# Kernel tuning notes

Measured on AMD Instinct MI355X. Metric: run time of the kernel, lower is better.

The kernel has to match this reference:

```python
import jax, jax.numpy as jnp
import numpy as np

NUM_HEADS = 32
NUM_KV_HEADS = 8
HEAD_DIM = 64
HIDDEN = 2048
EPS = 1e-05
ROPE_THETA = 1000000.0


def _rmsnorm(x, w):
    # x: [..., head_dim]
    var = jnp.mean(x * x, axis=-1, keepdims=True)
    return w * (x * jax.lax.rsqrt(var + EPS))


def _rope(q, k):
    # q,k: [B, h, T, d]
    T, d = q.shape[2], q.shape[3]
    inv_freq = 1.0 / (ROPE_THETA ** (jnp.arange(0, d, 2, dtype=jnp.float32) / d))
    t = jnp.arange(T, dtype=jnp.float32)
    freqs = jnp.outer(t, inv_freq)               # [T, d/2]
    emb = jnp.concatenate([freqs, freqs], -1)    # [T, d]
    cos = jnp.cos(emb)[None, None].astype(q.dtype)
    sin = jnp.sin(emb)[None, None].astype(q.dtype)

    def rotate(x):
        x1, x2 = x[..., : d // 2], x[..., d // 2 :]
        return jnp.concatenate([-x2, x1], -1)

    return q * cos + rotate(q) * sin, k * cos + rotate(k) * sin


def setup_inputs() -> dict:
    key = jax.random.key(0)
    ks = jax.random.split(key, 7)
    s = 0.02
    x = jax.random.normal(ks[0], (2, 2048, HIDDEN), jnp.float32)
    Wq = jax.random.normal(ks[1], (HIDDEN, NUM_HEADS * HEAD_DIM), jnp.float32) * s
    Wk = jax.random.normal(ks[2], (HIDDEN, NUM_KV_HEADS * HEAD_DIM), jnp.float32) * s
    Wv = jax.random.normal(ks[3], (HIDDEN, NUM_KV_HEADS * HEAD_DIM), jnp.float32) * s
    Wo = jax.random.normal(ks[4], (NUM_HEADS * HEAD_DIM, HIDDEN), jnp.float32) * s
    q_ln_w = jnp.ones((HEAD_DIM,), jnp.float32)
    k_ln_w = jnp.ones((HEAD_DIM,), jnp.float32)
    return {"x": x, "Wq": Wq, "Wk": Wk, "Wv": Wv, "Wo": Wo, "q_ln_w": q_ln_w, "k_ln_w": k_ln_w}


def reference(x, Wq, Wk, Wv, Wo, q_ln_w, k_ln_w):
    B, T, _ = x.shape
    g = NUM_HEADS // NUM_KV_HEADS  # GQA groups = 4
    q = (x @ Wq).reshape(B, T, NUM_HEADS, HEAD_DIM)
    k = (x @ Wk).reshape(B, T, NUM_KV_HEADS, HEAD_DIM)
    v = (x @ Wv).reshape(B, T, NUM_KV_HEADS, HEAD_DIM)
    q = _rmsnorm(q, q_ln_w)
    k = _rmsnorm(k, k_ln_w)
    q = q.transpose(0, 2, 1, 3)  # [B, nh, T, d]
    k = k.transpose(0, 2, 1, 3)  # [B, nkv, T, d]
    v = v.transpose(0, 2, 1, 3)
    q, k = _rope(q, k)
    # native GQA: fold query heads into (kv_head, group) without repeating K/V
    qg = q.reshape(B, NUM_KV_HEADS, g, T, HEAD_DIM)
    scale = 1.0 / jnp.sqrt(jnp.array(HEAD_DIM, q.dtype))
    scores = jnp.einsum("bkgtd,bksd->bkgts", qg, k) * scale  # [B,nkv,g,T,T]
    causal = jnp.tril(jnp.ones((T, T), bool))
    scores = jnp.where(causal, scores, jnp.finfo(scores.dtype).min)
    probs = jax.nn.softmax(scores, axis=-1)
    out = jnp.einsum("bkgts,bksd->bkgtd", probs, v)  # [B,nkv,g,T,d]
    out = out.reshape(B, NUM_HEADS, T, HEAD_DIM).transpose(0, 2, 1, 3).reshape(B, T, -1)
    return out @ Wo
```

## Files before the change

kernel.cpp:

```cpp
#include <hip/hip_runtime.h>
#include <cstdint>
#include <cstddef>

typedef unsigned short u16;
typedef __attribute__((ext_vector_type(8))) short short8;
typedef __attribute__((ext_vector_type(4))) short short4v;
typedef __attribute__((ext_vector_type(4))) float float4v;
typedef __attribute__((ext_vector_type(4))) unsigned short ushort4v;
typedef __attribute__((ext_vector_type(2))) float float2v;

__device__ __forceinline__ u16 f2bf(float f) {
    union { float f; uint32_t u; } x; x.f = f;
    uint32_t r = x.u + 0x7fffu + ((x.u >> 16) & 1u);
    return (u16)(r >> 16);
}
__device__ __forceinline__ float bf2f(u16 b) {
    union { uint32_t u; float f; } x; x.u = ((uint32_t)b) << 16;
    return x.f;
}
__device__ __forceinline__ uint32_t pack_bf16x2(float lo, float hi) {
    union { float f; uint32_t u; } a, b; a.f = lo; b.f = hi;
    return __builtin_amdgcn_perm(b.u + 0x8000u, a.u + 0x8000u, 0x07060302u);
}
__device__ __forceinline__ void gload_lds16(const u16* g, u16* l) {
    __builtin_amdgcn_global_load_lds(
        (const __attribute__((address_space(1))) void*)g,
        (__attribute__((address_space(3))) void*)l,
        16, 0, 0);
}

__global__ __launch_bounds__(256) void prep(const float4v* __restrict__ x,
                                            const float* __restrict__ Wq,
                                            const float* __restrict__ Wk,
                                            const float* __restrict__ Wv,
                                            const float* __restrict__ Wo,
                                            ushort4v* __restrict__ xb,
                                            u16* __restrict__ wqkv_t,
                                            u16* __restrict__ wo_t,
                                            float2v* __restrict__ tab) {
    __shared__ float lds[32][33];
    const int bid = blockIdx.x;
    const int tid = threadIdx.x;
    if (bid < 8192) {
        const int i = bid * 256 + tid;
        float4v v = x[i];
        ushort4v o;
        #pragma unroll
        for (int j = 0; j < 4; ++j) o[j] = f2bf(v[j]);
        xb[i] = o;
        return;
    }
    if (bid < 8448) {
        const int idx = (bid - 8192) * 256 + tid;
        const int t = idx >> 5;
        const int i = idx & 31;
        const float invf = exp2f(-(float)i * (19.931568569324174f / 32.0f));
        float sv, cv;
        sincosf((float)t * invf, &sv, &cv);
        float2v o; o[0] = cv; o[1] = sv;
        tab[idx] = o;
        return;
    }
    const float* src;
    int Ns, n0, k0, scol0;
    u16* dst;
    if (bid < 14592) {
        const int id = bid - 8448;
        const int bx = id % 96, by = id / 96;
        n0 = bx * 32; k0 = by * 32;
        if (n0 < 2048)      { src = Wq; Ns = 2048; scol0 = n0; }
        else if (n0 < 2560) { src = Wk; Ns = 512;  scol0 = n0 - 2048; }
        else                { src = Wv; Ns = 512;  scol0 = n0 - 2560; }
        dst = wqkv_t;
    } else {
        const int id = bid - 14592;
        const int bx = id & 63, by = id >> 6;
        n0 = bx * 32; k0 = by * 32;
        src = Wo; Ns = 2048; scol0 = n0;
        dst = wo_t;
    }
    const int row = tid >> 3;
    const int c4  = (tid & 7) * 4;
    const float4v v = *(const float4v*)(src + (size_t)(k0 + row) * Ns + scol0 + c4);
    #pragma unroll
    for (int i = 0; i < 4; ++i) lds[row][c4 + i] = v[i];
    __syncthreads();
    const int nrow = tid >> 3;
    const int k4   = (tid & 7) * 4;
    ushort4v o;
    #pragma unroll
    for (int i = 0; i < 4; ++i) o[i] = f2bf(lds[k4 + i][nrow]);
    *(ushort4v*)(dst + (size_t)(n0 + nrow) * 2048 + k0 + k4) = o;
}

__global__ __launch_bounds__(256) void gemm_bt(const u16* __restrict__ A,
                                               const u16* __restrict__ Bt,
                                               float* __restrict__ C,
                                               int M, int N, int K) {
    __shared__ u16 lds_a[128 * 32];
    __shared__ u16 lds_b[128 * 32];
    const int tid  = threadIdx.x;
    const int wave = tid >> 6;
    const int lane = tid & 63;
    const int quad = lane >> 4;
    const int l15  = lane & 15;
    const long m0 = (long)blockIdx.x * 128;
    const long n0 = (long)blockIdx.y * 128;
    const int wm = (wave >> 1) * 64;
    const int wn = (wave & 1) * 64;
    const int sa_row = lane >> 2;
    const int sa_col = (lane & 3) * 8;

    float4v acc[4][4];
    #pragma unroll
    for (int i = 0; i < 4; ++i)
        #pragma unroll
        for (int j = 0; j < 4; ++j)
            #pragma unroll
            for (int r = 0; r < 4; ++r) acc[i][j][r] = 0.0f;

    for (int k0 = 0; k0 < K; k0 += 32) {
        #pragma unroll
        for (int i = 0; i < 2; ++i) {
            const int slot = wave * 2 + i;
            const u16* ga = A  + (m0 + slot * 16 + sa_row) * (long)K + k0 + sa_col;
            gload_lds16(ga, lds_a + slot * 512);
            const u16* gb = Bt + (n0 + slot * 16 + sa_row) * (long)K + k0 + sa_col;
            gload_lds16(gb, lds_b + slot * 512);
        }
        __syncthreads();
        short8 af[4], bfr[4];
        #pragma unroll
        for (int mt = 0; mt < 4; ++mt)
            af[mt] = *(const short8*)(lds_a + (wm + mt * 16 + l15) * 32 + quad * 8);
        #pragma unroll
        for (int nt = 0; nt < 4; ++nt)
            bfr[nt] = *(const short8*)(lds_b + (wn + nt * 16 + l15) * 32 + quad * 8);
        #pragma unroll
        for (int mt = 0; mt < 4; ++mt)
            #pragma unroll
            for (int nt = 0; nt < 4; ++nt)
                acc[mt][nt] = __builtin_amdgcn_mfma_f32_16x16x32_bf16(af[mt], bfr[nt], acc[mt][nt], 0, 0, 0);
        __syncthreads();
    }
    #pragma unroll
    for (int mt = 0; mt < 4; ++mt) {
        #pragma unroll
        for (int nt = 0; nt < 4; ++nt) {
            const long gr = m0 + wm + mt * 16 + quad * 4;
            const long gc = n0 + wn + nt * 16 + l15;
            #pragma unroll
            for (int r = 0; r < 4; ++r)
                C[(gr + r) * N + gc] = acc[mt][nt][r];
        }
    }
}

__global__ __launch_bounds__(256) void gemm_qkv(const u16* __restrict__ A,
                                                const u16* __restrict__ Bt,
                                                const float* __restrict__ qw,
                                                const float* __restrict__ kw,
                                                const float2v* __restrict__ tab,
                                                u16* __restrict__ Qr,
                                                u16* __restrict__ Kr,
                                                u16* __restrict__ Vt) {
    const int K = 2048;
    __shared__ u16 lds_a[128 * 32];
    __shared__ u16 lds_b[128 * 32];
    const int tid  = threadIdx.x;
    const int wave = tid >> 6;
    const int lane = tid & 63;
    const int quad = lane >> 4;
    const int l15  = lane & 15;
    const long m0 = (long)blockIdx.x * 128;
    const long n0 = (long)blockIdx.y * 128;
    const int wm = (wave >> 1) * 64;
    const int wn = (wave & 1) * 64;
    const int sa_row = lane >> 2;
    const int sa_col = (lane & 3) * 8;

    float4v acc[4][4];
    #pragma unroll
    for (int i = 0; i < 4; ++i)
        #pragma unroll
        for (int j = 0; j < 4; ++j)
            #pragma unroll
            for (int r = 0; r < 4; ++r) acc[i][j][r] = 0.0f;

    for (int k0 = 0; k0 < K; k0 += 32) {
        #pragma unroll
        for (int i = 0; i < 2; ++i) {
            const int slot = wave * 2 + i;
            const u16* ga = A  + (m0 + slot * 16 + sa_row) * (long)K + k0 + sa_col;
            gload_lds16(ga, lds_a + slot * 512);
            const u16* gb = Bt + (n0 + slot * 16 + sa_row) * (long)K + k0 + sa_col;
            gload_lds16(gb, lds_b + slot * 512);
        }
        __syncthreads();
        short8 af[4], bfr[4];
        #pragma unroll
        for (int mt = 0; mt < 4; ++mt)
            af[mt] = *(const short8*)(lds_a + (wm + mt * 16 + l15) * 32 + quad * 8);
        #pragma unroll
        for (int nt = 0; nt < 4; ++nt)
            bfr[nt] = *(const short8*)(lds_b + (wn + nt * 16 + l15) * 32 + quad * 8);
        #pragma unroll
        for (int mt = 0; mt < 4; ++mt)
            #pragma unroll
            for (int nt = 0; nt < 4; ++nt)
                acc[mt][nt] = __builtin_amdgcn_mfma_f32_16x16x32_bf16(af[mt], bfr[nt], acc[mt][nt], 0, 0, 0);
        __syncthreads();
    }

    const int col0 = (int)n0 + wn;
    if (col0 < 2560) {
        const bool isQ = (col0 < 2048);
        const float* lw = isQ ? qw : kw;
        float wreg[4];
        #pragma unroll
        for (int nt = 0; nt < 4; ++nt) wreg[nt] = lw[nt * 16 + l15];
        const float qs = isQ ? 0.18033688011112042f : 1.0f;
        u16* dst = isQ ? (Qr + ((size_t)(col0 >> 6)) * 2048 * 64)
                       : (Kr + ((size_t)((col0 - 2048) >> 6)) * 2048 * 64);
        const size_t head_stride = isQ ? ((size_t)32 * 2048 * 64) : ((size_t)8 * 2048 * 64);
        #pragma unroll
        for (int mt = 0; mt < 4; ++mt) {
            const int gr0 = (int)m0 + wm + mt * 16 + quad * 4;
            const int b = gr0 >> 11, tt0 = gr0 & 2047;
            float rms[4];
            #pragma unroll
            for (int r = 0; r < 4; ++r) {
                float s = 0.0f;
                #pragma unroll
                for (int nt = 0; nt < 4; ++nt) s += acc[mt][nt][r] * acc[mt][nt][r];
                s += __shfl_xor(s, 1);
                s += __shfl_xor(s, 2);
                s += __shfl_xor(s, 4);
                s += __shfl_xor(s, 8);
                rms[r] = rsqrtf(s * (1.0f / 64.0f) + 1e-5f);
            }
            u16* rowp = dst + (size_t)b * head_stride + (size_t)tt0 * 64;
            #pragma unroll
            for (int nt = 0; nt < 2; ++nt) {
                const int i = nt * 16 + l15;
                #pragma unroll
                for (int r = 0; r < 4; ++r) {
                    const float2v cs = tab[(tt0 + r) * 32 + i];
                    const float v1 = acc[mt][nt][r]     * rms[r] * wreg[nt];
                    const float v2 = acc[mt][nt + 2][r] * rms[r] * wreg[nt + 2];
                    const float o1 = (v1 * cs[0] - v2 * cs[1]) * qs;
                    const float o2 = (v2 * cs[0] + v1 * cs[1]) * qs;
                    rowp[(size_t)r * 64 + i]      = f2bf(o1);
                    rowp[(size_t)r * 64 + i + 32] = f2bf(o2);
                }
            }
        }
    } else {
        const int kh = (col0 - 2560) >> 6;
        #pragma unroll
        for (int mt = 0; mt < 4; ++mt) {
            const int gr0 = (int)m0 + wm + mt * 16 + quad * 4;
            const int b = gr0 >> 11, tt0 = gr0 & 2047;
            #pragma unroll
            for (int nt = 0; nt < 4; ++nt) {
                const int d = nt * 16 + l15;
                ushort4v o;
                #pragma unroll
                for (int r = 0; r < 4; ++r) o[r] = f2bf(acc[mt][nt][r]);
                *(ushort4v*)(Vt + (((size_t)(b * 8 + kh)) * 64 + d) * 2048 + tt0) = o;
            }
        }
    }
}

#define KSTR 72
#define VSTR 136
__global__ __launch_bounds__(512, 4) void attn_fwd(const u16* __restrict__ Qr,
                                                   const u16* __restrict__ Kr,
                                                   const u16* __restrict__ Vt,
                                                   u16* __restrict__ Ob) {
    __shared__ u16 lds_k[2][128 * KSTR];
    __shared__ u16 lds_vt[2][64 * VSTR];
    const int tid  = threadIdx.x;
    const int wave = tid >> 6;
    const int lane = tid & 63;
    const int quad = lane >> 4;
    const int l15  = lane & 15;
    const int qxB = blockIdx.x;
    const int qxA = 15 - qxB;
    const int bh = blockIdx.y;
    const int b = bh >> 5, h = bh & 31;
    const int kh = h >> 2;
    const u16* Qh = Qr + ((size_t)(b * 32 + h))  * 2048 * 64;
    const u16* Kh = Kr + ((size_t)(b * 8 + kh))  * 2048 * 64;
    const u16* Vh = Vt + ((size_t)(b * 8 + kh))  * 64 * 2048;

    const int k_key0 = tid >> 3;
    const int k_d0   = (tid & 7) * 8;
    const int v_d0   = tid >> 4;
    const int v_k8   = (tid & 15) * 8;

    const int qrowA = qxA * 128 + wave * 16 + l15;
    const int qrowB = qxB * 128 + wave * 16 + l15;
    short8 qfA[2], qfB[2];
    #pragma unroll
    for (int ks = 0; ks < 2; ++ks) {
        qfA[ks] = *(const short8*)(Qh + (size_t)qrowA * 64 + ks * 32 + quad * 8);
        qfB[ks] = *(const short8*)(Qh + (size_t)qrowB * 64 + ks * 32 + quad * 8);
    }
    short8 qf0 = qfA[0], qf1 = qfA[1];
    int qrow_cur = qrowA;

    float m_i = -3e38f, l_i = 0.0f;
    float4v Oacc[4];
    #pragma unroll
    for (int dt = 0; dt < 4; ++dt)
        #pragma unroll
        for (int r = 0; r < 4; ++r) Oacc[dt][r] = 0.0f;

    short8 kreg[2], vreg[2];
    #pragma unroll
    for (int i = 0; i < 2; ++i) {
        kreg[i] = *(const short8*)(Kh + (size_t)(k_key0 + i * 64) * 64 + k_d0);
        vreg[i] = *(const short8*)(Vh + (size_t)(v_d0 + i * 32) * 2048 + v_k8);
    }
    #pragma unroll
    for (int i = 0; i < 2; ++i) {
        *(short8*)(lds_k[0]  + (k_key0 + i * 64) * KSTR + k_d0) = kreg[i];
        *(short8*)(lds_vt[0] + (v_d0 + i * 32) * VSTR + v_k8)   = vreg[i];
    }
    __syncthreads();

    const int n_it = 17;
    for (int i = 0; i < n_it; ++i) {
        const int p = i & 1;
        const bool last = (i == n_it - 1);
        const int kt_cur = (i <= qxA) ? i : (i - qxA - 1);
        const int kt0 = kt_cur << 7;

        if (!last) {
            const int ip1 = i + 1;
            const int ktn = (ip1 <= qxA) ? ip1 : (ip1 - qxA - 1);
            const size_t nk0 = (size_t)(ktn << 7);
            #pragma unroll
            for (int j = 0; j < 2; ++j) {
                kreg[j] = *(const short8*)(Kh + (nk0 + k_key0 + j * 64) * 64 + k_d0);
                vreg[j] = *(const short8*)(Vh + (size_t)(v_d0 + j * 32) * 2048 + nk0 + v_k8);
            }
        }

        float4v S[8];
        #pragma unroll
        for (int nt = 0; nt < 8; ++nt)
            #pragma unroll
            for (int r = 0; r < 4; ++r) S[nt][r] = 0.0f;
        #pragma unroll
        for (int ks = 0; ks < 2; ++ks) {
            const short8 qf = ks ? qf1 : qf0;
            #pragma unroll
            for (int nt = 0; nt < 8; ++nt) {
                short8 kf = *(const short8*)(lds_k[p] + (nt * 16 + l15) * KSTR + ks * 32 + quad * 8);
                S[nt] = __builtin_amdgcn_mfma_f32_16x16x32_bf16(kf, qf, S[nt], 0, 0, 0);
            }
        }
        if (i == qxA || last) {
            #pragma unroll
            for (int nt = 0; nt < 8; ++nt) {
                const int keyb = kt0 + nt * 16 + quad * 4;
                #pragma unroll
                for (int r = 0; r < 4; ++r)
                    if (keyb + r > qrow_cur) S[nt][r] = -3e38f;
            }
        }
        float mx = S[0][0];
        #pragma unroll
        for (int nt = 0; nt < 8; ++nt)
            #pragma unroll
            for (int r = 0; r < 4; ++r) mx = fmaxf(mx, S[nt][r]);
        mx = fmaxf(mx, __shfl_xor(mx, 16));
        mx = fmaxf(mx, __shfl_xor(mx, 32));
        const float mnew = fmaxf(m_i, mx);
        const float alpha = __builtin_amdgcn_exp2f(m_i - mnew);
        m_i = mnew;
        float rs = 0.0f;
        #pragma unroll
        for (int nt = 0; nt < 8; ++nt)
            #pragma unroll
            for (int r = 0; r < 4; ++r) {
                const float pv = __builtin_amdgcn_exp2f(S[nt][r] - mnew);
                S[nt][r] = pv;
                rs += pv;
            }
        rs += __shfl_xor(rs, 16);
        rs += __shfl_xor(rs, 32);
        l_i = l_i * alpha + rs;
        #pragma unroll
        for (int dt = 0; dt < 4; ++dt)
            #pragma unroll
            for (int r = 0; r < 4; ++r) Oacc[dt][r] *= alpha;

        #pragma unroll
        for (int nt = 0; nt < 8; ++nt) {
            union { uint32_t u[2]; short4v s; } pu;
            pu.u[0] = pack_bf16x2(S[nt][0], S[nt][1]);
            pu.u[1] = pack_bf16x2(S[nt][2], S[nt][3]);
            const short4v pf = pu.s;
            #pragma unroll
            for (int dt = 0; dt < 4; ++dt) {
                const short4v vf = *(const short4v*)(lds_vt[p] + (dt * 16 + l15) * VSTR + nt * 16 + quad * 4);
                Oacc[dt] = __builtin_amdgcn_mfma_f32_16x16x16bf16_1k(vf, pf, Oacc[dt], 0, 0, 0);
            }
        }

        if (i == qxA) {
            const float rl = 1.0f / l_i;
            #pragma unroll
            for (int dt = 0; dt < 4; ++dt) {
                ushort4v o;
                #pragma unroll
                for (int r = 0; r < 4; ++r) o[r] = f2bf(Oacc[dt][r] * rl);
                *(ushort4v*)(Ob + ((size_t)(b * 2048 + qrowA)) * 2048 + h * 64 + dt * 16 + quad * 4) = o;
            }
            m_i = -3e38f;
            l_i = 0.0f;
            qf0 = qfB[0];
            qf1 = qfB[1];
            qrow_cur = qrowB;
        }

        if (!last) {
            #pragma unroll
            for (int j = 0; j < 2; ++j) {
                *(short8*)(lds_k[1 - p]  + (k_key0 + j * 64) * KSTR + k_d0) = kreg[j];
                *(short8*)(lds_vt[1 - p] + (v_d0 + j * 32) * VSTR + v_k8)   = vreg[j];
            }
        }
        __syncthreads();
    }
    const float rl = 1.0f / l_i;
    #pragma unroll
    for (int dt = 0; dt < 4; ++dt) {
        ushort4v o;
        #pragma unroll
        for (int r = 0; r < 4; ++r) o[r] = f2bf(Oacc[dt][r] * rl);
        *(ushort4v*)(Ob + ((size_t)(b * 2048 + qrowB)) * 2048 + h * 64 + dt * 16 + quad * 4) = o;
    }
}

extern "C" void kernel_launch(void* const* d_in, const int* in_sizes, int n_in,
                              void* d_out, int out_size, void* d_ws, size_t ws_size,
                              hipStream_t stream) {
    (void)in_sizes; (void)n_in; (void)out_size; (void)ws_size;
    const float* x  = (const float*)d_in[0];
    const float* Wq = (const float*)d_in[1];
    const float* Wk = (const float*)d_in[2];
    const float* Wv = (const float*)d_in[3];
    const float* Wo = (const float*)d_in[4];
    const float* qw = (const float*)d_in[5];
    const float* kw = (const float*)d_in[6];
    float* out = (float*)d_out;

    char* ws = (char*)d_ws;
    size_t off = 0;
    auto alloc = [&](size_t bytes) {
        char* p = ws + off;
        off += (bytes + 255) & ~(size_t)255;
        return p;
    };
    u16* xb     = (u16*)alloc((size_t)8388608 * 2);
    u16* wqkv_t = (u16*)alloc((size_t)3072 * 2048 * 2);
    u16* wo_t   = (u16*)alloc((size_t)2048 * 2048 * 2);
    u16* q_r    = (u16*)alloc((size_t)2 * 32 * 2048 * 64 * 2);
    u16* k_r    = (u16*)alloc((size_t)2 * 8 * 2048 * 64 * 2);
    u16* v_r    = (u16*)alloc((size_t)2 * 8 * 64 * 2048 * 2);
    float2v* rtab = (float2v*)alloc((size_t)2048 * 32 * 8);
    u16* attnb  = xb;

    hipLaunchKernelGGL(prep, dim3(18688), dim3(256), 0, stream,
                       (const float4v*)x, Wq, Wk, Wv, Wo,
                       (ushort4v*)xb, wqkv_t, wo_t, rtab);
    hipLaunchKernelGGL(gemm_qkv, dim3(32, 24), dim3(256), 0, stream,
                       xb, wqkv_t, qw, kw, rtab, q_r, k_r, v_r);
    hipLaunchKernelGGL(attn_fwd, dim3(8, 64), dim3(512), 0, stream, q_r, k_r, v_r, attnb);
    hipLaunchKernelGGL(gemm_bt, dim3(32, 16), dim3(256), 0, stream,
                       attnb, wo_t, out, 4096, 2048, 2048);
}
```

Measured before the change: 331.1 us.

## Double-buffer GEMM LDS tiles with register prefetch instead of direct global-to-LDS loads

Both the output-projection GEMM and the fused QKV GEMM now keep two LDS buffers per operand. The next K-tile is loaded into registers while MFMAs run on the current buffer, then written to the other buffer, so there is one barrier per iteration instead of two. This is meant to hide global load latency behind compute. It replaces the direct global_load_lds path with register staging, which costs more VGPRs and doubles LDS use, and it adds a launch-bounds occupancy hint of 3.

```diff
diff --git a/kernel.cpp b/kernel.cpp
--- a/kernel.cpp
+++ b/kernel.cpp
@@ -14,19 +14,9 @@
     uint32_t r = x.u + 0x7fffu + ((x.u >> 16) & 1u);
     return (u16)(r >> 16);
 }
-__device__ __forceinline__ float bf2f(u16 b) {
-    union { uint32_t u; float f; } x; x.u = ((uint32_t)b) << 16;
-    return x.f;
-}
 __device__ __forceinline__ uint32_t pack_bf16x2(float lo, float hi) {
     union { float f; uint32_t u; } a, b; a.f = lo; b.f = hi;
     return __builtin_amdgcn_perm(b.u + 0x8000u, a.u + 0x8000u, 0x07060302u);
-}
-__device__ __forceinline__ void gload_lds16(const u16* g, u16* l) {
-    __builtin_amdgcn_global_load_lds(
-        (const __attribute__((address_space(1))) void*)g,
-        (__attribute__((address_space(3))) void*)l,
-        16, 0, 0);
 }
 
 __global__ __launch_bounds__(256) void prep(const float4v* __restrict__ x,
@@ -93,12 +83,12 @@
     *(ushort4v*)(dst + (size_t)(n0 + nrow) * 2048 + k0 + k4) = o;
 }
 
-__global__ __launch_bounds__(256) void gemm_bt(const u16* __restrict__ A,
-                                               const u16* __restrict__ Bt,
-                                               float* __restrict__ C,
-                                               int M, int N, int K) {
-    __shared__ u16 lds_a[128 * 32];
-    __shared__ u16 lds_b[128 * 32];
+__global__ __launch_bounds__(256, 3) void gemm_bt(const u16* __restrict__ A,
+                                                  const u16* __restrict__ Bt,
+                                                  float* __restrict__ C,
+                                                  int M, int N, int K) {
+    __shared__ u16 lds_a[2][128 * 32];
+    __shared__ u16 lds_b[2][128 * 32];
     const int tid  = threadIdx.x;
     const int wave = tid >> 6;
     const int lane = tid & 63;
@@ -108,8 +98,8 @@
     const long n0 = (long)blockIdx.y * 128;
     const int wm = (wave >> 1) * 64;
     const int wn = (wave & 1) * 64;
-    const int sa_row = lane >> 2;
-    const int sa_col = (lane & 3) * 8;
+    const int s_row = tid >> 2;
+    const int s_col = (tid & 3) * 8;
 
     float4v acc[4][4];
     #pragma unroll
@@ -119,28 +109,49 @@
             #pragma unroll
             for (int r = 0; r < 4; ++r) acc[i][j][r] = 0.0f;
 
-    for (int k0 = 0; k0 < K; k0 += 32) {
-        #pragma unroll
-        for (int i = 0; i < 2; ++i) {
-            const int slot = wave * 2 + i;
-            const u16* ga = A  + (m0 + slot * 16 + sa_row) * (long)K + k0 + sa_col;
-            gload_lds16(ga, lds_a + slot * 512);
-            const u16* gb = Bt + (n0 + slot * 16 + sa_row) * (long)K + k0 + sa_col;
-            gload_lds16(gb, lds_b + slot * 512);
-        }
-        __syncthreads();
+    short8 areg[2], breg[2];
+    #pragma unroll
+    for (int c = 0; c < 2; ++c) {
+        areg[c] = *(const short8*)(A  + (m0 + c * 64 + s_row) * (long)K + s_col);
+        breg[c] = *(const short8*)(Bt + (n0 + c * 64 + s_row) * (long)K + s_col);
+    }
+    #pragma unroll
+    for (int c = 0; c < 2; ++c) {
+        *(short8*)(lds_a[0] + (c * 64 + s_row) * 32 + s_col) = areg[c];
+        *(short8*)(lds_b[0] + (c * 64 + s_row) * 32 + s_col) = breg[c];
+    }
+    __syncthreads();
+
+    const int n_k = K >> 5;
+    for (int it = 0; it < n_k; ++it) {
+        const int p = it & 1;
+        if (it + 1 < n_k) {
+            const int kn = (it + 1) << 5;
+            #pragma unroll
+            for (int c = 0; c < 2; ++c) {
+                areg[c] = *(const short8*)(A  + (m0 + c * 64 + s_row) * (long)K + kn + s_col);
+                breg[c] = *(const short8*)(Bt + (n0 + c * 64 + s_row) * (long)K + kn + s_col);
+            }
+        }
         short8 af[4], bfr[4];
         #pragma unroll
         for (int mt = 0; mt < 4; ++mt)
-            af[mt] = *(const short8*)(lds_a + (wm + mt * 16 + l15) * 32 + quad * 8);
+            af[mt] = *(const short8*)(lds_a[p] + (wm + mt * 16 + l15) * 32 + quad * 8);
         #pragma unroll
         for (int nt = 0; nt < 4; ++nt)
-            bfr[nt] = *(const short8*)(lds_b + (wn + nt * 16 + l15) * 32 + quad * 8);
+            bfr[nt] = *(const short8*)(lds_b[p] + (wn + nt * 16 + l15) * 32 + quad * 8);
         #pragma unroll
         for (int mt = 0; mt < 4; ++mt)
             #pragma unroll
             for (int nt = 0; nt < 4; ++nt)
                 acc[mt][nt] = __builtin_amdgcn_mfma_f32_16x16x32_bf16(af[mt], bfr[nt], acc[mt][nt], 0, 0, 0);
+        if (it + 1 < n_k) {
+            #pragma unroll
+            for (int c = 0; c < 2; ++c) {
+                *(short8*)(lds_a[1 - p] + (c * 64 + s_row) * 32 + s_col) = areg[c];
+                *(short8*)(lds_b[1 - p] + (c * 64 + s_row) * 32 + s_col) = breg[c];
+            }
+        }
         __syncthreads();
     }
     #pragma unroll
@@ -156,17 +167,17 @@
     }
 }
 
-__global__ __launch_bounds__(256) void gemm_qkv(const u16* __restrict__ A,
-                                                const u16* __restrict__ Bt,
-                                                const float* __restrict__ qw,
-                                                const float* __restrict__ kw,
-                                                const float2v* __restrict__ tab,
-                                                u16* __restrict__ Qr,
-                                                u16* __restrict__ Kr,
-                                                u16* __restrict__ Vt) {
+__global__ __launch_bounds__(256, 3) void gemm_qkv(const u16* __restrict__ A,
+                                                   const u16* __restrict__ Bt,
+                                                   const float* __restrict__ qw,
+                                                   const float* __restrict__ kw,
+                                                   const float2v* __restrict__ tab,
+                                                   u16* __restrict__ Qr,
+                                                   u16* __restrict__ Kr,
+                                                   u16* __restrict__ Vt) {
     const int K = 2048;
-    __shared__ u16 lds_a[128 * 32];
-    __shared__ u16 lds_b[128 * 32];
+    __shared__ u16 lds_a[2][128 * 32];
+    __shared__ u16 lds_b[2][128 * 32];
     const int tid  = threadIdx.x;
     const int wave = tid >> 6;
     const int lane = tid & 63;
@@ -176,8 +187,8 @@
     const long n0 = (long)blockIdx.y * 128;
     const int wm = (wave >> 1) * 64;
     const int wn = (wave & 1) * 64;
-    const int sa_row = lane >> 2;
-    const int sa_col = (lane & 3) * 8;
+    const int s_row = tid >> 2;
+    const int s_col = (tid & 3) * 8;
 
     float4v acc[4][4];
     #pragma unroll
@@ -187,28 +198,49 @@
             #pragma unroll
             for (int r = 0; r < 4; ++r) acc[i][j][r] = 0.0f;
 
-    for (int k0 = 0; k0 < K; k0 += 32) {
-        #pragma unroll
-        for (int i = 0; i < 2; ++i) {
-            const int slot = wave * 2 + i;
-            const u16* ga = A  + (m0 + slot * 16 + sa_row) * (long)K + k0 + sa_col;
-            gload_lds16(ga, lds_a + slot * 512);
-            const u16* gb = Bt + (n0 + slot * 16 + sa_row) * (long)K + k0 + sa_col;
-            gload_lds16(gb, lds_b + slot * 512);
-        }
-        __syncthreads();
+    short8 areg[2], breg[2];
+    #pragma unroll
+    for (int c = 0; c < 2; ++c) {
+        areg[c] = *(const short8*)(A  + (m0 + c * 64 + s_row) * (long)K + s_col);
+        breg[c] = *(const short8*)(Bt + (n0 + c * 64 + s_row) * (long)K + s_col);
+    }
+    #pragma unroll
+    for (int c = 0; c < 2; ++c) {
+        *(short8*)(lds_a[0] + (c * 64 + s_row) * 32 + s_col) = areg[c];
+        *(short8*)(lds_b[0] + (c * 64 + s_row) * 32 + s_col) = breg[c];
+    }
+    __syncthreads();
+
+    const int n_k = K >> 5;
+    for (int it = 0; it < n_k; ++it) {
+        const int p = it & 1;
+        if (it + 1 < n_k) {
+            const int kn = (it + 1) << 5;
+            #pragma unroll
+            for (int c = 0; c < 2; ++c) {
+                areg[c] = *(const short8*)(A  + (m0 + c * 64 + s_row) * (long)K + kn + s_col);
+                breg[c] = *(const short8*)(Bt + (n0 + c * 64 + s_row) * (long)K + kn + s_col);
+            }
+        }
         short8 af[4], bfr[4];
         #pragma unroll
         for (int mt = 0; mt < 4; ++mt)
-            af[mt] = *(const short8*)(lds_a + (wm + mt * 16 + l15) * 32 + quad * 8);
+            af[mt] = *(const short8*)(lds_a[p] + (wm + mt * 16 + l15) * 32 + quad * 8);
         #pragma unroll
         for (int nt = 0; nt < 4; ++nt)
-            bfr[nt] = *(const short8*)(lds_b + (wn + nt * 16 + l15) * 32 + quad * 8);
+            bfr[nt] = *(const short8*)(lds_b[p] + (wn + nt * 16 + l15) * 32 + quad * 8);
         #pragma unroll
         for (int mt = 0; mt < 4; ++mt)
             #pragma unroll
             for (int nt = 0; nt < 4; ++nt)
                 acc[mt][nt] = __builtin_amdgcn_mfma_f32_16x16x32_bf16(af[mt], bfr[nt], acc[mt][nt], 0, 0, 0);
+        if (it + 1 < n_k) {
+            #pragma unroll
+            for (int c = 0; c < 2; ++c) {
+                *(short8*)(lds_a[1 - p] + (c * 64 + s_row) * 32 + s_col) = areg[c];
+                *(short8*)(lds_b[1 - p] + (c * 64 + s_row) * 32 + s_col) = breg[c];
+            }
+        }
         __syncthreads();
     }
 
```

After: 299.7 us. -9.5%, faster.
